# Kernel optimization log

Measured on AMD Instinct MI355X. Metric: run time of the kernel, lower is better.

Reference implementation:

```python
import jax, jax.numpy as jnp
import numpy as np
import math

B, Q, C, H, L, P = 8, 900, 256, 8, 4, 4
D = C // H  # head_dim = 32
SPATIAL = np.array([[100, 100], [50, 50], [25, 25], [13, 13]], dtype=np.int64)
AREAS = SPATIAL[:, 0] * SPATIAL[:, 1]
STARTS = np.concatenate([[0], np.cumsum(AREAS)[:-1]]).astype(np.int64)
S = int(AREAS.sum())  # 13294


def _xavier(k, i, o, scale=1.0):
    return jax.random.normal(k, (i, o), jnp.float32) * scale * (2.0 / (i + o)) ** 0.5


def setup_inputs() -> dict:
    key = jax.random.key(0)
    ks = jax.random.split(key, 16)
    inp = {}
    inp['query'] = jax.random.normal(ks[0], (B, Q, C), jnp.float32)
    inp['reference_points'] = jax.random.uniform(ks[1], (B, Q, L, 2), jnp.float32)
    inp['input_flatten'] = jax.random.normal(ks[2], (B, S, C), jnp.float32)
    inp['object_shape'] = jax.random.uniform(ks[3], (B, Q, 2), jnp.float32) * 0.3 + 0.02
    inp['input_spatial_shapes'] = jnp.asarray(SPATIAL)
    inp['input_level_start_index'] = jnp.asarray(STARTS)
    # learned parameters (torch zero-inits offset/attn weights; use small random for a nontrivial baseline)
    inp['w_q'] = _xavier(ks[4], C, C); inp['b_q'] = jnp.zeros((C,), jnp.float32)
    inp['w_v'] = _xavier(ks[5], C, C); inp['b_v'] = jnp.zeros((C,), jnp.float32)
    inp['w_o'] = _xavier(ks[6], C, C); inp['b_o'] = jnp.zeros((C,), jnp.float32)
    inp['w_off1'] = _xavier(ks[7], C + 2, C); inp['b_off1'] = jnp.zeros((C,), jnp.float32)
    inp['w_off2'] = _xavier(ks[8], C, H * L * P * 2, scale=0.05)
    inp['b_off2'] = jax.random.normal(ks[9], (H * L * P * 2,), jnp.float32) * 0.02
    inp['w_ax'] = _xavier(ks[10], C, H * L * P, scale=0.1); inp['b_ax'] = jnp.zeros((H * L * P,), jnp.float32)
    inp['w_ay'] = _xavier(ks[11], C, H * L * P, scale=0.1); inp['b_ay'] = jnp.zeros((H * L * P,), jnp.float32)
    # spectral basis per original init: head h uses freq pi*(h+1)/H over arange(D)
    freq = (np.arange(1, H + 1, dtype=np.float32)[:, None] * math.pi / H) * np.arange(D, dtype=np.float32)[None, :]
    inp['basis_x'] = jnp.asarray(np.cos(freq), jnp.float32)
    inp['basis_y'] = jnp.asarray(np.sin(freq), jnp.float32)
    return inp


def _bilinear_sample(v, locs):
    """v: (B,S,H,D); locs: (B,Q,H,L,P,2) in [0,1]. grid_sample semantics: align_corners=False, zeros padding.
    Returns (B,Q,H,L,P,D)."""
    levels = []
    for lvl in range(L):
        Hl, Wl = int(SPATIAL[lvl, 0]), int(SPATIAL[lvl, 1])
        start = int(STARTS[lvl])
        v_l = v[:, start:start + Hl * Wl]  # (B, Hl*Wl, H, D)
        loc = locs[:, :, :, lvl]  # (B,Q,H,P,2)
        # align_corners=False: pixel coord = loc * size - 0.5
        x = loc[..., 0] * Wl - 0.5
        y = loc[..., 1] * Hl - 0.5
        x0 = jnp.floor(x); y0 = jnp.floor(y)
        fx = x - x0; fy = y - y0
        x0i = x0.astype(jnp.int32); y0i = y0.astype(jnp.int32)
        acc = jnp.zeros((B, Q, H, P, D), jnp.float32)
        corners = [(0, 0, (1 - fx) * (1 - fy)), (1, 0, fx * (1 - fy)),
                   (0, 1, (1 - fx) * fy), (1, 1, fx * fy)]
        for dx, dy, w in corners:
            xi = x0i + dx; yi = y0i + dy
            valid = (xi >= 0) & (xi < Wl) & (yi >= 0) & (yi < Hl)
            idx = jnp.clip(yi, 0, Hl - 1) * Wl + jnp.clip(xi, 0, Wl - 1)  # (B,Q,H,P)
            idx_t = idx.transpose(0, 1, 3, 2).reshape(B, Q * P, H)[..., None]  # (B,Q*P,H,1)
            g = jnp.take_along_axis(v_l, idx_t, axis=1)  # (B,Q*P,H,D)
            g = g.reshape(B, Q, P, H, D).transpose(0, 1, 3, 2, 4)  # (B,Q,H,P,D)
            acc = acc + g * (w * valid.astype(jnp.float32))[..., None]
        levels.append(acc)
    return jnp.stack(levels, axis=3)  # (B,Q,H,L,P,D)


def reference(query, reference_points, input_flatten, input_spatial_shapes, input_level_start_index,
              object_shape, w_q, b_q, w_v, b_v, w_o, b_o, w_off1, b_off1, w_off2, b_off2,
              w_ax, b_ax, w_ay, b_ay, basis_x, basis_y):
    q = query @ w_q + b_q  # (B,Q,C)
    v = (input_flatten @ w_v + b_v).reshape(B, S, H, D)
    q_shape = jnp.concatenate([q, object_shape], axis=-1)  # (B,Q,C+2)
    hid = jax.nn.relu(q_shape @ w_off1 + b_off1)
    offsets = (hid @ w_off2 + b_off2).reshape(B, Q, H, L, P, 2)
    offsets = offsets * object_shape[:, :, None, None, None, :]
    ref = reference_points[:, :, None, :, None, :]  # (B,Q,1,L,1,2)
    locs = jnp.clip(ref + offsets, 0.0, 1.0)  # (B,Q,H,L,P,2)
    q_heads = q.reshape(B, Q, H, D)
    spec = jnp.einsum('bqhd,hd->bqh', q_heads, basis_x) * jnp.einsum('bqhd,hd->bqh', q_heads, basis_y)
    attn_x = (q @ w_ax + b_ax).reshape(B, Q, H, L, P)
    attn_y = (q @ w_ay + b_ay).reshape(B, Q, H, L, P)
    attn = attn_x * attn_y + spec[..., None, None]
    attn = jax.nn.softmax(attn.reshape(B, Q, H, L * P), axis=-1).reshape(B, Q, H, L, P)
    sampled = _bilinear_sample(v, locs)  # (B,Q,H,L,P,D)
    out = (sampled * attn[..., None]).sum(axis=(3, 4)).reshape(B, Q, C)
    return out @ w_o + b_o  # dropout is identity in eval
```

## Files before the change

### kernel.cpp

```cpp
#include <hip/hip_runtime.h>
#include <hip/hip_bf16.h>
#include <math.h>

constexpr int B_ = 8, Q_ = 900;
constexpr int S_ = 13294;
constexpr int BQ = 7200;
constexpr int BS = 106352;
constexpr int NVB = 831;

typedef __bf16 bf16x8 __attribute__((ext_vector_type(8)));
typedef float  f32x4  __attribute__((ext_vector_type(4)));

#define WAITLGKM0 asm volatile("s_waitcnt lgkmcnt(0)" ::: "memory")
#define SCHEDB    __builtin_amdgcn_sched_barrier(0)
#define BAR       __builtin_amdgcn_s_barrier()
#define CFENCE    asm volatile("" ::: "memory")

__device__ __forceinline__ void load_lds16(const void* g, void* lds) {
    __builtin_amdgcn_global_load_lds(
        (const __attribute__((address_space(1))) void*)g,
        (__attribute__((address_space(3))) void*)lds, 16, 0, 0);
}

__device__ __forceinline__ float wcat_f(const float* __restrict__ wax,
                                        const float* __restrict__ way,
                                        const float* __restrict__ woff1,
                                        int c, int n)
{
    if (n < 128) return wax[(size_t)c * 128 + n];
    if (n < 256) return way[(size_t)c * 128 + (n - 128)];
    return woff1[(size_t)c * 256 + (n - 256)];
}

__global__ __launch_bounds__(256)
void prep_all(const float* __restrict__ wv, const float* __restrict__ wo,
              const float* __restrict__ woff2, const float* __restrict__ wq,
              const float* __restrict__ wax, const float* __restrict__ way,
              const float* __restrict__ woff1, const float* __restrict__ bq,
              const float* __restrict__ bax, const float* __restrict__ bay,
              const float* __restrict__ boff1,
              __bf16* __restrict__ tv, __bf16* __restrict__ to_,
              __bf16* __restrict__ toff2, __bf16* __restrict__ wcomb,
              float* __restrict__ bcomb)
{
    const int bi = blockIdx.x;
    __shared__ float tile[32][33];

    if (bi < 192) {
        const int wid = bi >> 6, t = bi & 63;
        const int k0 = (t & 7) * 32, n0 = (t >> 3) * 32;
        const int tx = threadIdx.x & 31, ty = threadIdx.x >> 5;
        const float* src; __bf16* dst;
        if      (wid == 0) { src = wv;    dst = tv;    }
        else if (wid == 1) { src = wo;    dst = to_;   }
        else               { src = woff2; dst = toff2; }
        #pragma unroll
        for (int i = 0; i < 4; ++i)
            tile[ty + 8 * i][tx] = src[(size_t)(k0 + ty + 8 * i) * 256 + n0 + tx];
        __syncthreads();
        #pragma unroll
        for (int i = 0; i < 4; ++i)
            dst[(size_t)(n0 + ty + 8 * i) * 256 + k0 + tx] = (__bf16)tile[tx][ty + 8 * i];
        return;
    }

    if (bi >= 200) {
        const int n = (bi - 200) * 256 + threadIdx.x;
        float acc = (n < 128) ? bax[n] : (n < 256 ? bay[n - 128] : boff1[n - 256]);
        for (int c = 0; c < 256; ++c)
            acc += bq[c] * (float)(__bf16)wcat_f(wax, way, woff1, c, n);
        bcomb[n] = acc;
        return;
    }

    const int wid  = ((bi - 192) << 2) + (threadIdx.x >> 6);
    const int lane = threadIdx.x & 63;
    const int n0 = (wid >> 2) * 64, k0 = (wid & 3) * 64;
    const int l15 = lane & 15, l4 = lane >> 4;

    f32x4 acc[4][4] = {};
    #pragma unroll
    for (int s = 0; s < 8; ++s) {
        const int c0 = s * 32 + l4 * 8;
        bf16x8 am[4], bm[4];
        #pragma unroll
        for (int mi = 0; mi < 4; ++mi) {
            const int n = n0 + mi * 16 + l15;
            #pragma unroll
            for (int j = 0; j < 8; ++j)
                am[mi][j] = (__bf16)wcat_f(wax, way, woff1, c0 + j, n);
        }
        #pragma unroll
        for (int ni = 0; ni < 4; ++ni) {
            const float* wr_ = wq + (size_t)(k0 + ni * 16 + l15) * 256 + c0;
            const float4 f0 = ((const float4*)wr_)[0];
            const float4 f1 = ((const float4*)wr_)[1];
            bm[ni][0] = (__bf16)f0.x; bm[ni][1] = (__bf16)f0.y;
            bm[ni][2] = (__bf16)f0.z; bm[ni][3] = (__bf16)f0.w;
            bm[ni][4] = (__bf16)f1.x; bm[ni][5] = (__bf16)f1.y;
            bm[ni][6] = (__bf16)f1.z; bm[ni][7] = (__bf16)f1.w;
        }
        #pragma unroll
        for (int mi = 0; mi < 4; ++mi)
            #pragma unroll
            for (int ni = 0; ni < 4; ++ni)
                acc[mi][ni] = __builtin_amdgcn_mfma_f32_16x16x32_bf16(
                    am[mi], bm[ni], acc[mi][ni], 0, 0, 0);
    }
    #pragma unroll
    for (int mi = 0; mi < 4; ++mi)
        #pragma unroll
        for (int rr = 0; rr < 4; ++rr) {
            const int n = n0 + mi * 16 + l4 * 4 + rr;
            #pragma unroll
            for (int ni = 0; ni < 4; ++ni)
                wcomb[(size_t)n * 256 + k0 + ni * 16 + l15] = (__bf16)acc[mi][ni][rr];
        }
}

__global__ __launch_bounds__(512)
void main_fused(const float* __restrict__ x_in, const __bf16* __restrict__ wt_v,
                const float* __restrict__ b_v, __bf16* __restrict__ v_bf,
                const float* __restrict__ query, const __bf16* __restrict__ wcomb,
                const float* __restrict__ bcomb, const float* __restrict__ objs,
                const float* __restrict__ wex, float* __restrict__ axyhid)
{
    __shared__ float4 AsbV[2][512];
    __shared__ float4 BsbV[3][1024];
    char* const Asb_b = (char*)AsbV;
    char* const Bsb_b = (char*)BsbV;

    const int bid  = blockIdx.x;
    const bool isV = (bid < NVB);
    const int qb   = bid - NVB;
    const int colhalf = isV ? 0 : (qb & 1);

    const float*  A    = isV ? x_in : query;
    const __bf16* Wt   = isV ? wt_v : (wcomb + (size_t)colhalf * 256 * 256);
    const float*  bias = isV ? b_v  : (bcomb + colhalf * 256);
    const int     M    = isV ? BS   : BQ;
    const int     row0 = isV ? bid * 128 : (qb >> 1) * 128;

    const int tid  = threadIdx.x;
    const int wave = tid >> 6, lane = tid & 63;
    const int wr = wave >> 2, wc = wave & 3;
    const int l15 = lane & 15, l4 = lane >> 4;

    const int st_row = tid >> 2, st_kq = tid & 3;
    const int gr_cl  = min(row0 + st_row, M - 1);
    const float* Abase = A + (size_t)gr_cl * 256 + st_kq * 8;
    const int a_wo = st_row * 64 + ((st_kq ^ ((st_row >> 1) & 3)) * 16);

    int a_off[4], b_off[4];
    #pragma unroll
    for (int mi = 0; mi < 4; ++mi) {
        const int r = wr * 64 + mi * 16 + l15;
        a_off[mi] = r * 64 + (l4 ^ ((r >> 1) & 3)) * 16;
    }
    #pragma unroll
    for (int ni = 0; ni < 4; ++ni) {
        const int c = wc * 64 + ni * 16 + l15;
        b_off[ni] = c * 64 + (l4 ^ ((c >> 1) & 3)) * 16;
    }

    const __bf16* bsrc[2];
    #pragma unroll
    for (int i = 0; i < 2; ++i) {
        const int c   = (wave * 2 + i) * 64 + lane;
        const int col = c >> 2, kcp = c & 3;
        const int kc  = kcp ^ ((col >> 1) & 3);
        bsrc[i] = Wt + (size_t)col * 256 + kc * 8;
    }

    auto issueB = [&](int kt, int bbuf) {
        #pragma unroll
        for (int i = 0; i < 2; ++i)
            load_lds16(bsrc[i] + kt * 32, Bsb_b + bbuf * 16384 + (wave * 2 + i) * 1024);
    };
    auto loadA = [&](int kt, float4* g) {
        const float* ga = Abase + kt * 32;
        g[0] = ((const float4*)ga)[0];
        g[1] = ((const float4*)ga)[1];
    };
    auto writeA = [&](int abuf, const float4* g) {
        bf16x8 c0;
        c0[0] = (__bf16)g[0].x; c0[1] = (__bf16)g[0].y; c0[2] = (__bf16)g[0].z; c0[3] = (__bf16)g[0].w;
        c0[4] = (__bf16)g[1].x; c0[5] = (__bf16)g[1].y; c0[6] = (__bf16)g[1].z; c0[7] = (__bf16)g[1].w;
        *(bf16x8*)(Asb_b + abuf * 8192 + a_wo) = c0;
    };

    f32x4 acc[4][4] = {};
    float4 g[2][2];

    issueB(0, 0);
    loadA(0, g[0]);
    issueB(1, 1);
    loadA(1, g[1]);
    writeA(0, g[0]);
    WAITLGKM0; BAR; CFENCE; SCHEDB;

    #pragma unroll
    for (int u = 0; u < 8; ++u) {
        if (u + 2 <= 7) {
            loadA(u + 2, g[u & 1]);
            issueB(u + 2, (u + 2) % 3);
        }

        if (u < 6)       { asm volatile("s_waitcnt vmcnt(8)" ::: "memory"); }
        else if (u == 6) { asm volatile("s_waitcnt vmcnt(4)" ::: "memory"); }
        else             { asm volatile("s_waitcnt vmcnt(0)" ::: "memory"); }
        SCHEDB;

        const char* Ab = Asb_b + (u & 1) * 8192;
        const char* Bb = Bsb_b + (u % 3) * 16384;
        bf16x8 a[4], b[4];
        #pragma unroll
        for (int mi = 0; mi < 4; ++mi) a[mi] = *(const bf16x8*)(Ab + a_off[mi]);
        #pragma unroll
        for (int ni = 0; ni < 4; ++ni) b[ni] = *(const bf16x8*)(Bb + b_off[ni]);

        #pragma unroll
        for (int mi = 0; mi < 4; ++mi)
            #pragma unroll
            for (int ni = 0; ni < 4; ++ni)
                acc[mi][ni] = __builtin_amdgcn_mfma_f32_16x16x32_bf16(
                    a[mi], b[ni], acc[mi][ni], 0, 0, 0);

        if (u + 1 <= 7) {
            writeA((u + 1) & 1, g[(u + 1) & 1]);
            WAITLGKM0; BAR; CFENCE; SCHEDB;
        }
    }

    float bb[4];
    #pragma unroll
    for (int ni = 0; ni < 4; ++ni) bb[ni] = bias[wc * 64 + ni * 16 + l15];

    if (isV) {
        #pragma unroll
        for (int mi = 0; mi < 4; ++mi)
            #pragma unroll
            for (int rr = 0; rr < 4; ++rr) {
                const int row = row0 + wr * 64 + mi * 16 + l4 * 4 + rr;
                if (row >= M) continue;
                #pragma unroll
                for (int ni = 0; ni < 4; ++ni)
                    v_bf[(size_t)row * 256 + wc * 64 + ni * 16 + l15] =
                        (__bf16)(acc[mi][ni][rr] + bb[ni]);
            }
    } else {
        float we0[4], we1[4];
        #pragma unroll
        for (int ni = 0; ni < 4; ++ni) {
            const int c = wc * 64 + ni * 16 + l15;
            we0[ni] = colhalf ? wex[c]       : 0.f;
            we1[ni] = colhalf ? wex[256 + c] : 0.f;
        }
        #pragma unroll
        for (int mi = 0; mi < 4; ++mi)
            #pragma unroll
            for (int rr = 0; rr < 4; ++rr) {
                const int row = row0 + wr * 64 + mi * 16 + l4 * 4 + rr;
                if (row >= M) continue;
                const float e0 = objs[(size_t)row * 2];
                const float e1 = objs[(size_t)row * 2 + 1];
                #pragma unroll
                for (int ni = 0; ni < 4; ++ni) {
                    const int c = wc * 64 + ni * 16 + l15;
                    float v = acc[mi][ni][rr] + bb[ni];
                    if (colhalf) {
                        v += e0 * we0[ni] + e1 * we1[ni];
                        v = fmaxf(v, 0.f);
                    }
                    axyhid[(size_t)row * 512 + colhalf * 256 + c] = v;
                }
            }
    }
}

template<bool OUTBF16>
__global__ __launch_bounds__(256)
void gemm_dp(const float* __restrict__ A, const __bf16* __restrict__ Wt,
             const float* __restrict__ bias, void* __restrict__ outp,
             int M, int N, int LDA)
{
    __shared__ float4 AsbV[2][512];
    __shared__ float4 BsbV[3][512];
    char* const Asb_b = (char*)AsbV;
    char* const Bsb_b = (char*)BsbV;

    const int tid  = threadIdx.x;
    const int wave = tid >> 6, lane = tid & 63;
    const int wr = wave >> 1, wc = wave & 1;
    const int row0 = blockIdx.y * 128, col0 = blockIdx.x * 128;
    const int l15 = lane & 15, l4 = lane >> 4;

    const int st_row = tid >> 1, st_kh = tid & 1;
    const int gr_cl  = min(row0 + st_row, M - 1);
    const float* Abase = A + (size_t)gr_cl * LDA + st_kh * 16;
    const int asw   = (st_row >> 1) & 3;
    const int a_wo0 = st_row * 64 + ((st_kh * 2)     ^ asw) * 16;
    const int a_wo1 = st_row * 64 + ((st_kh * 2 + 1) ^ asw) * 16;

    int a_off[4], b_off[4];
    #pragma unroll
    for (int mi = 0; mi < 4; ++mi) {
        const int r   = wr * 64 + mi * 16 + l15;
        a_off[mi] = r * 64 + (l4 ^ ((r >> 1) & 3)) * 16;
    }
    #pragma unroll
    for (int ni = 0; ni < 4; ++ni) {
        const int c   = wc * 64 + ni * 16 + l15;
        b_off[ni] = c * 64 + (l4 ^ ((c >> 1) & 3)) * 16;
    }

    const __bf16* bsrc[2];
    #pragma unroll
    for (int i = 0; i < 2; ++i) {
        const int c   = (wave * 2 + i) * 64 + lane;
        const int col = c >> 2, kcp = c & 3;
        const int kc  = kcp ^ ((col >> 1) & 3);
        bsrc[i] = Wt + (size_t)(col0 + col) * 256 + kc * 8;
    }

    auto issueB = [&](int kt, int bbuf) {
        #pragma unroll
        for (int i = 0; i < 2; ++i)
            load_lds16(bsrc[i] + kt * 32, Bsb_b + bbuf * 8192 + (wave * 2 + i) * 1024);
    };
    auto loadA = [&](int kt, float4* g) {
        const float* ga = Abase + kt * 32;
        g[0] = ((const float4*)ga)[0];
        g[1] = ((const float4*)ga)[1];
        g[2] = ((const float4*)ga)[2];
        g[3] = ((const float4*)ga)[3];
    };
    auto writeA = [&](int abuf, const float4* g) {
        bf16x8 c0, c1;
        c0[0] = (__bf16)g[0].x; c0[1] = (__bf16)g[0].y; c0[2] = (__bf16)g[0].z; c0[3] = (__bf16)g[0].w;
        c0[4] = (__bf16)g[1].x; c0[5] = (__bf16)g[1].y; c0[6] = (__bf16)g[1].z; c0[7] = (__bf16)g[1].w;
        c1[0] = (__bf16)g[2].x; c1[1] = (__bf16)g[2].y; c1[2] = (__bf16)g[2].z; c1[3] = (__bf16)g[2].w;
        c1[4] = (__bf16)g[3].x; c1[5] = (__bf16)g[3].y; c1[6] = (__bf16)g[3].z; c1[7] = (__bf16)g[3].w;
        *(bf16x8*)(Asb_b + abuf * 8192 + a_wo0) = c0;
        *(bf16x8*)(Asb_b + abuf * 8192 + a_wo1) = c1;
    };

    f32x4 acc[4][4] = {};
    float4 g[2][4];

    issueB(0, 0);
    loadA(0, g[0]);
    issueB(1, 1);
    loadA(1, g[1]);
    writeA(0, g[0]);
    WAITLGKM0; BAR; CFENCE; SCHEDB;

    #pragma unroll
    for (int u = 0; u < 8; ++u) {
        if (u + 2 <= 7) {
            loadA(u + 2, g[u & 1]);
            issueB(u + 2, (u + 2) % 3);
        }

        if (u < 6)       { asm volatile("s_waitcnt vmcnt(12)" ::: "memory"); }
        else if (u == 6) { asm volatile("s_waitcnt vmcnt(6)" ::: "memory"); }
        else             { asm volatile("s_waitcnt vmcnt(0)" ::: "memory"); }
        SCHEDB;

        const char* Ab = Asb_b + (u & 1) * 8192;
        const char* Bb = Bsb_b + (u % 3) * 8192;
        bf16x8 a[4], b[4];
        #pragma unroll
        for (int mi = 0; mi < 4; ++mi) a[mi] = *(const bf16x8*)(Ab + a_off[mi]);
        #pragma unroll
        for (int ni = 0; ni < 4; ++ni) b[ni] = *(const bf16x8*)(Bb + b_off[ni]);

        #pragma unroll
        for (int mi = 0; mi < 4; ++mi)
            #pragma unroll
            for (int ni = 0; ni < 4; ++ni)
                acc[mi][ni] = __builtin_amdgcn_mfma_f32_16x16x32_bf16(
                    a[mi], b[ni], acc[mi][ni], 0, 0, 0);

        if (u + 1 <= 7) {
            writeA((u + 1) & 1, g[(u + 1) & 1]);
            WAITLGKM0; BAR; CFENCE; SCHEDB;
        }
    }

    float bb[4];
    #pragma unroll
    for (int ni = 0; ni < 4; ++ni) bb[ni] = bias[col0 + wc * 64 + ni * 16 + l15];
    #pragma unroll
    for (int mi = 0; mi < 4; ++mi) {
        #pragma unroll
        for (int rr = 0; rr < 4; ++rr) {
            const int row = row0 + wr * 64 + mi * 16 + l4 * 4 + rr;
            if (row >= M) continue;
            #pragma unroll
            for (int ni = 0; ni < 4; ++ni) {
                const float v = acc[mi][ni][rr] + bb[ni];
                const int colb = col0 + wc * 64 + ni * 16 + l15;
                if (OUTBF16) ((__bf16*)outp)[(size_t)row * N + colb] = (__bf16)v;
                else         ((float*)outp)[(size_t)row * N + colb]  = v;
            }
        }
    }
}

__global__ __launch_bounds__(256)
void attn_sample_kernel(const float* __restrict__ axyhid,
                        const float* __restrict__ refp, const float* __restrict__ objs,
                        const float* __restrict__ off, const __bf16* __restrict__ v,
                        float* __restrict__ agg)
{
    const int bq = blockIdx.x;
    const int b  = bq / Q_;
    const int tid = threadIdx.x;

    __shared__ float sm[128];
    __shared__ float sa[128];
    __shared__ float sl[256];

    if (tid < 128)
        sm[tid] = axyhid[(size_t)bq * 512 + tid] * axyhid[(size_t)bq * 512 + 128 + tid];
    __syncthreads();

    if (tid < 128) {
        const int hh = tid >> 4;
        float mx = -1e30f;
        #pragma unroll
        for (int i = 0; i < 16; ++i) mx = fmaxf(mx, sm[hh * 16 + i]);
        float s = 0.f;
        #pragma unroll
        for (int i = 0; i < 16; ++i) s += __expf(sm[hh * 16 + i] - mx);
        sa[tid] = __expf(sm[tid] - mx) / s;

        const int l = (tid >> 2) & 3;
        const float os0 = objs[(size_t)bq * 2], os1 = objs[(size_t)bq * 2 + 1];
        const float r0 = refp[((size_t)bq * 4 + l) * 2];
        const float r1 = refp[((size_t)bq * 4 + l) * 2 + 1];
        const float o0 = off[(size_t)bq * 256 + tid * 2]     * os0;
        const float o1 = off[(size_t)bq * 256 + tid * 2 + 1] * os1;
        sl[tid * 2]     = fminf(fmaxf(r0 + o0, 0.f), 1.f);
        sl[tid * 2 + 1] = fminf(fmaxf(r1 + o1, 0.f), 1.f);
    }
    __syncthreads();

    const int h = tid >> 5, lane32 = tid & 31;
    const int sp = lane32 >> 2, cq = lane32 & 3;
    const int chbase = h * 32 + cq * 8;
    const __bf16* vb = v + (size_t)b * S_ * 256;

    float acc8[8] = {};

    #pragma unroll
    for (int gidx = 0; gidx < 2; ++gidx) {
        const int lp  = gidx * 8 + sp;
        const int li  = h * 16 + lp;
        const int lvl = lp >> 2;
        const int Wl = (lvl == 0) ? 100 : (lvl == 1) ? 50 : (lvl == 2) ? 25 : 13;
        const int Hl = Wl;
        const int st = (lvl == 0) ? 0 : (lvl == 1) ? 10000 : (lvl == 2) ? 12500 : 13125;

        const float a  = sa[li];
        const float lx = sl[li * 2], ly = sl[li * 2 + 1];
        const float x = lx * (float)Wl - 0.5f;
        const float y = ly * (float)Hl - 0.5f;
        const float x0f = floorf(x), y0f = floorf(y);
        const float fx = x - x0f, fy = y - y0f;
        const int x0 = (int)x0f, y0 = (int)y0f;

        #pragma unroll
        for (int c = 0; c < 4; ++c) {
            const int dx = c & 1, dy = c >> 1;
            const int xi = x0 + dx, yi = y0 + dy;
            const float wgt = (dx ? fx : 1.f - fx) * (dy ? fy : 1.f - fy);
            const bool valid = (xi >= 0) & (xi < Wl) & (yi >= 0) & (yi < Hl);
            const int idx = min(max(yi, 0), Hl - 1) * Wl + min(max(xi, 0), Wl - 1);
            const float wa = valid ? a * wgt : 0.f;
            const bf16x8 gv = *(const bf16x8*)(vb + (size_t)(st + idx) * 256 + chbase);
            #pragma unroll
            for (int j = 0; j < 8; ++j) acc8[j] += wa * (float)gv[j];
        }
    }

    #pragma unroll
    for (int m = 4; m <= 16; m <<= 1)
        #pragma unroll
        for (int j = 0; j < 8; ++j)
            acc8[j] += __shfl_xor(acc8[j], m);

    if (sp == 0) {
        #pragma unroll
        for (int j = 0; j < 8; ++j)
            agg[(size_t)bq * 256 + chbase + j] = acc8[j];
    }
}

extern "C" void kernel_launch(void* const* d_in, const int* in_sizes, int n_in,
                              void* d_out, int out_size, void* d_ws, size_t ws_size,
                              hipStream_t stream)
{
    const float* query = (const float*)d_in[0];
    const float* refp  = (const float*)d_in[1];
    const float* x_in  = (const float*)d_in[2];
    const float* objs  = (const float*)d_in[3];
    const float* w_q    = (const float*)d_in[6];
    const float* b_q    = (const float*)d_in[7];
    const float* w_v    = (const float*)d_in[8];
    const float* b_v    = (const float*)d_in[9];
    const float* w_o    = (const float*)d_in[10];
    const float* b_o    = (const float*)d_in[11];
    const float* w_off1 = (const float*)d_in[12];
    const float* b_off1 = (const float*)d_in[13];
    const float* w_off2 = (const float*)d_in[14];
    const float* b_off2 = (const float*)d_in[15];
    const float* w_ax   = (const float*)d_in[16];
    const float* b_ax   = (const float*)d_in[17];
    const float* w_ay   = (const float*)d_in[18];
    const float* b_ay   = (const float*)d_in[19];

    float* ws = (float*)d_ws;
    float* axyhid_ws = ws;
    float* off_ws    = axyhid_ws + (size_t)BQ * 512;
    float* agg_ws    = off_ws    + (size_t)BQ * 256;
    float* bcomb_ws  = agg_ws    + (size_t)BQ * 256;
    __bf16* v_bf    = (__bf16*)(bcomb_ws + 512);
    __bf16* wt_v    = v_bf    + (size_t)BS * 256;
    __bf16* wt_o    = wt_v    + 256 * 256;
    __bf16* wt_off2 = wt_o    + 256 * 256;
    __bf16* wcomb   = wt_off2 + 256 * 256;

    const dim3 blk(256);

    prep_all<<<202, blk, 0, stream>>>(w_v, w_o, w_off2, w_q, w_ax, w_ay, w_off1,
                                      b_q, b_ax, b_ay, b_off1,
                                      wt_v, wt_o, wt_off2, wcomb, bcomb_ws);

    main_fused<<<NVB + 114, dim3(512), 0, stream>>>(
        x_in, wt_v, b_v, v_bf,
        query, wcomb, bcomb_ws, objs, w_off1 + 256 * 256, axyhid_ws);

    gemm_dp<false><<<dim3(2, (BQ + 127) / 128), blk, 0, stream>>>(
        axyhid_ws + 256, wt_off2, b_off2, off_ws, BQ, 256, 512);

    attn_sample_kernel<<<BQ, blk, 0, stream>>>(axyhid_ws, refp, objs, off_ws,
                                               v_bf, agg_ws);

    gemm_dp<false><<<dim3(2, (BQ + 127) / 128), blk, 0, stream>>>(
        agg_ws, wt_o, b_o, (float*)d_out, BQ, 256, 256);
}
```

Measured before the change: 108.9 us.

## Restructure main fused GEMM to 256 threads with 128x64 per-wave tiles

The fused V/query projection GEMM kernel moves from 512 threads (8 waves, 2x4 layout, 64x64 per wave) to 256 threads (4 waves, each covering all 128 rows and 64 columns) with launch bounds allowing two blocks per CU. Each thread now stages twice as much A and B data per k-step, and the vmcnt waits are adjusted to match. The aim is better A-fragment reuse per wave and fewer waves per block, at the cost of doubled accumulator registers (128 floats) per thread, which may limit occupancy or cause spills.

Result: slower. 114.9 us (+5.5%).

```diff
diff --git a/kernel.cpp b/kernel.cpp
--- a/kernel.cpp
+++ b/kernel.cpp
@@ -118,7 +118,7 @@
         }
 }
 
-__global__ __launch_bounds__(512)
+__global__ __launch_bounds__(256, 2)
 void main_fused(const float* __restrict__ x_in, const __bf16* __restrict__ wt_v,
                 const float* __restrict__ b_v, __bf16* __restrict__ v_bf,
                 const float* __restrict__ query, const __bf16* __restrict__ wcomb,
@@ -143,30 +143,31 @@
 
     const int tid  = threadIdx.x;
     const int wave = tid >> 6, lane = tid & 63;
-    const int wr = wave >> 2, wc = wave & 3;
     const int l15 = lane & 15, l4 = lane >> 4;
 
-    const int st_row = tid >> 2, st_kq = tid & 3;
+    const int st_row = tid >> 1, st_kh = tid & 1;
     const int gr_cl  = min(row0 + st_row, M - 1);
-    const float* Abase = A + (size_t)gr_cl * 256 + st_kq * 8;
-    const int a_wo = st_row * 64 + ((st_kq ^ ((st_row >> 1) & 3)) * 16);
-
-    int a_off[4], b_off[4];
-    #pragma unroll
-    for (int mi = 0; mi < 4; ++mi) {
-        const int r = wr * 64 + mi * 16 + l15;
+    const float* Abase = A + (size_t)gr_cl * 256 + st_kh * 16;
+    const int asw   = (st_row >> 1) & 3;
+    const int a_wo0 = st_row * 64 + ((st_kh * 2)     ^ asw) * 16;
+    const int a_wo1 = st_row * 64 + ((st_kh * 2 + 1) ^ asw) * 16;
+
+    int a_off[8], b_off[4];
+    #pragma unroll
+    for (int mi = 0; mi < 8; ++mi) {
+        const int r = mi * 16 + l15;
         a_off[mi] = r * 64 + (l4 ^ ((r >> 1) & 3)) * 16;
     }
     #pragma unroll
     for (int ni = 0; ni < 4; ++ni) {
-        const int c = wc * 64 + ni * 16 + l15;
+        const int c = wave * 64 + ni * 16 + l15;
         b_off[ni] = c * 64 + (l4 ^ ((c >> 1) & 3)) * 16;
     }
 
-    const __bf16* bsrc[2];
-    #pragma unroll
-    for (int i = 0; i < 2; ++i) {
-        const int c   = (wave * 2 + i) * 64 + lane;
+    const __bf16* bsrc[4];
+    #pragma unroll
+    for (int i = 0; i < 4; ++i) {
+        const int c   = wave * 256 + i * 64 + lane;
         const int col = c >> 2, kcp = c & 3;
         const int kc  = kcp ^ ((col >> 1) & 3);
         bsrc[i] = Wt + (size_t)col * 256 + kc * 8;
@@ -174,23 +175,29 @@
 
     auto issueB = [&](int kt, int bbuf) {
         #pragma unroll
-        for (int i = 0; i < 2; ++i)
-            load_lds16(bsrc[i] + kt * 32, Bsb_b + bbuf * 16384 + (wave * 2 + i) * 1024);
+        for (int i = 0; i < 4; ++i)
+            load_lds16(bsrc[i] + kt * 32,
+                       Bsb_b + bbuf * 16384 + wave * 4096 + i * 1024);
     };
     auto loadA = [&](int kt, float4* g) {
         const float* ga = Abase + kt * 32;
         g[0] = ((const float4*)ga)[0];
         g[1] = ((const float4*)ga)[1];
+        g[2] = ((const float4*)ga)[2];
+        g[3] = ((const float4*)ga)[3];
     };
     auto writeA = [&](int abuf, const float4* g) {
-        bf16x8 c0;
+        bf16x8 c0, c1;
         c0[0] = (__bf16)g[0].x; c0[1] = (__bf16)g[0].y; c0[2] = (__bf16)g[0].z; c0[3] = (__bf16)g[0].w;
         c0[4] = (__bf16)g[1].x; c0[5] = (__bf16)g[1].y; c0[6] = (__bf16)g[1].z; c0[7] = (__bf16)g[1].w;
-        *(bf16x8*)(Asb_b + abuf * 8192 + a_wo) = c0;
+        c1[0] = (__bf16)g[2].x; c1[1] = (__bf16)g[2].y; c1[2] = (__bf16)g[2].z; c1[3] = (__bf16)g[2].w;
+        c1[4] = (__bf16)g[3].x; c1[5] = (__bf16)g[3].y; c1[6] = (__bf16)g[3].z; c1[7] = (__bf16)g[3].w;
+        *(bf16x8*)(Asb_b + abuf * 8192 + a_wo0) = c0;
+        *(bf16x8*)(Asb_b + abuf * 8192 + a_wo1) = c1;
     };
 
-    f32x4 acc[4][4] = {};
-    float4 g[2][2];
+    f32x4 acc[8][4] = {};
+    float4 g[2][4];
 
     issueB(0, 0);
     loadA(0, g[0]);
@@ -206,21 +213,21 @@
             issueB(u + 2, (u + 2) % 3);
         }
 
-        if (u < 6)       { asm volatile("s_waitcnt vmcnt(8)" ::: "memory"); }
-        else if (u == 6) { asm volatile("s_waitcnt vmcnt(4)" ::: "memory"); }
-        else             { asm volatile("s_waitcnt vmcnt(0)" ::: "memory"); }
+        if (u < 6)       { asm volatile("s_waitcnt vmcnt(16)" ::: "memory"); }
+        else if (u == 6) { asm volatile("s_waitcnt vmcnt(8)"  ::: "memory"); }
+        else             { asm volatile("s_waitcnt vmcnt(0)"  ::: "memory"); }
         SCHEDB;
 
         const char* Ab = Asb_b + (u & 1) * 8192;
         const char* Bb = Bsb_b + (u % 3) * 16384;
-        bf16x8 a[4], b[4];
-        #pragma unroll
-        for (int mi = 0; mi < 4; ++mi) a[mi] = *(const bf16x8*)(Ab + a_off[mi]);
+        bf16x8 a[8], b[4];
+        #pragma unroll
+        for (int mi = 0; mi < 8; ++mi) a[mi] = *(const bf16x8*)(Ab + a_off[mi]);
         #pragma unroll
         for (int ni = 0; ni < 4; ++ni) b[ni] = *(const bf16x8*)(Bb + b_off[ni]);
 
         #pragma unroll
-        for (int mi = 0; mi < 4; ++mi)
+        for (int mi = 0; mi < 8; ++mi)
             #pragma unroll
             for (int ni = 0; ni < 4; ++ni)
                 acc[mi][ni] = __builtin_amdgcn_mfma_f32_16x16x32_bf16(
@@ -234,39 +241,39 @@
 
     float bb[4];
     #pragma unroll
-    for (int ni = 0; ni < 4; ++ni) bb[ni] = bias[wc * 64 + ni * 16 + l15];
+    for (int ni = 0; ni < 4; ++ni) bb[ni] = bias[wave * 64 + ni * 16 + l15];
 
     if (isV) {
         #pragma unroll
-        for (int mi = 0; mi < 4; ++mi)
+        for (int mi = 0; mi < 8; ++mi)
             #pragma unroll
             for (int rr = 0; rr < 4; ++rr) {
-                const int row = row0 + wr * 64 + mi * 16 + l4 * 4 + rr;
+                const int row = row0 + mi * 16 + l4 * 4 + rr;
                 if (row >= M) continue;
                 #pragma unroll
                 for (int ni = 0; ni < 4; ++ni)
-                    v_bf[(size_t)row * 256 + wc * 64 + ni * 16 + l15] =
+                    v_bf[(size_t)row * 256 + wave * 64 + ni * 16 + l15] =
                         (__bf16)(acc[mi][ni][rr] + bb[ni]);
             }
     } else {
         float we0[4], we1[4];
         #pragma unroll
         for (int ni = 0; ni < 4; ++ni) {
-            const int c = wc * 64 + ni * 16 + l15;
+            const int c = wave * 64 + ni * 16 + l15;
             we0[ni] = colhalf ? wex[c]       : 0.f;
             we1[ni] = colhalf ? wex[256 + c] : 0.f;
         }
         #pragma unroll
-        for (int mi = 0; mi < 4; ++mi)
+        for (int mi = 0; mi < 8; ++mi)
             #pragma unroll
             for (int rr = 0; rr < 4; ++rr) {
-                const int row = row0 + wr * 64 + mi * 16 + l4 * 4 + rr;
+                const int row = row0 + mi * 16 + l4 * 4 + rr;
                 if (row >= M) continue;
                 const float e0 = objs[(size_t)row * 2];
                 const float e1 = objs[(size_t)row * 2 + 1];
                 #pragma unroll
                 for (int ni = 0; ni < 4; ++ni) {
-                    const int c = wc * 64 + ni * 16 + l15;
+                    const int c = wave * 64 + ni * 16 + l15;
                     float v = acc[mi][ni][rr] + bb[ni];
                     if (colhalf) {
                         v += e0 * we0[ni] + e1 * we1[ni];
@@ -538,7 +545,7 @@
                                       b_q, b_ax, b_ay, b_off1,
                                       wt_v, wt_o, wt_off2, wcomb, bcomb_ws);
 
-    main_fused<<<NVB + 114, dim3(512), 0, stream>>>(
+    main_fused<<<NVB + 114, blk, 0, stream>>>(
         x_in, wt_v, b_v, v_bf,
         query, wcomb, bcomb_ws, objs, w_off1 + 256 * 256, axyhid_ws);
 
```
